# Kernel optimization log

Measured on AMD Instinct MI355X. Metric: run time of the kernel, lower is better.

The kernel has to match this reference:

```python
import jax, jax.numpy as jnp
import numpy as np

B, S, D, P, L, V, C = 8, 4096, 512, 128, 4, 32000, 2
DF = 4 * D      # MLP hidden
DH = D // 2     # head hidden
EPS_LN = 1e-5
EPS_ATTN = 1e-6


def setup_inputs() -> dict:
    key = jax.random.key(0)
    ks = iter(jax.random.split(key, 32))

    def w(shape, fan_in):
        return jax.random.normal(next(ks), shape, jnp.float32) / np.sqrt(fan_in)

    inp = {
        "x": jax.random.randint(next(ks), (B, S), 0, V),
        "embed": jax.random.normal(next(ks), (V, D), jnp.float32) * 0.02,
        "pos": jax.random.normal(next(ks), (S, D), jnp.float32) * 0.02,
        # per-layer params, stacked on leading L axis
        "Wq": w((L, D, D), D), "bq": jnp.zeros((L, D), jnp.float32),
        "Wk": w((L, D, D), D), "bk": jnp.zeros((L, D), jnp.float32),
        "Wv": w((L, D, D), D), "bv": jnp.zeros((L, D), jnp.float32),
        "Wf": w((L, D, P), D), "bf": jnp.zeros((L, P), jnp.float32),
        "Wo": w((L, D, D), D), "bo": jnp.zeros((L, D), jnp.float32),
        "ln_g": jnp.ones((L, D), jnp.float32), "ln_b": jnp.zeros((L, D), jnp.float32),
        "W1": w((L, D, DF), D), "b1": jnp.zeros((L, DF), jnp.float32),
        "W2": w((L, DF, D), DF), "b2": jnp.zeros((L, D), jnp.float32),
        # head
        "Wh1": w((D, DH), D), "bh1": jnp.zeros((DH,), jnp.float32),
        "Wh2": w((DH, C), DH), "bh2": jnp.zeros((C,), jnp.float32),
    }
    return inp


def _layernorm(x, g, b):
    mu = x.mean(-1, keepdims=True)
    var = ((x - mu) ** 2).mean(-1, keepdims=True)
    return (x - mu) * jax.lax.rsqrt(var + EPS_LN) * g + b


def _linear_attn(h, Wq, bq, Wk, bk, Wv, bv, Wf, bf, Wo, bo):
    q = h @ Wq + bq
    k = h @ Wk + bk
    v = h @ Wv + bv
    # positive feature map (Performer-style kernelization) -> [B,S,P]
    pq = jax.nn.elu(q @ Wf + bf) + 1.0
    pk = jax.nn.elu(k @ Wf + bf) + 1.0
    kv = jnp.einsum('bsp,bsd->bpd', pk, v)              # [B,P,D]
    z = jnp.einsum('bsp,bp->bs', pq, pk.sum(axis=1))    # [B,S]
    out = jnp.einsum('bsp,bpd->bsd', pq, kv) / (z[..., None] + EPS_ATTN)
    return out @ Wo + bo


def reference(x, embed, pos, Wq, bq, Wk, bk, Wv, bv, Wf, bf, Wo, bo,
              ln_g, ln_b, W1, b1, W2, b2, Wh1, bh1, Wh2, bh2):
    h = embed[x] + pos[: x.shape[1]]                    # [B,S,D]
    for i in range(L):
        a = _linear_attn(h, Wq[i], bq[i], Wk[i], bk[i], Wv[i], bv[i],
                         Wf[i], bf[i], Wo[i], bo[i])
        a = _layernorm(a, ln_g[i], ln_b[i])
        m = jax.nn.gelu(a @ W1[i] + b1[i])              # [B,S,4D]
        h = m @ W2[i] + b2[i]
    pooled = h.mean(axis=1)                             # [B,D]
    h1 = jax.nn.relu(pooled @ Wh1 + bh1)
    return h1 @ Wh2 + bh2                               # [B,C]
```

## Files before the change

### kernel.cpp

```cpp
#include <hip/hip_runtime.h>

#define B_  8
#define S_  4096
#define D_  512
#define P_  128
#define L_  4
#define DF_ 2048
#define DH_ 256
#define C_  2
#define MTOT (B_*S_)
#define KC_ 8

typedef unsigned short u16;
typedef unsigned int   u32;
typedef short s8v __attribute__((ext_vector_type(8)));
typedef float f4v __attribute__((ext_vector_type(4)));

__device__ __forceinline__ float bf2f(u16 u) {
    return __uint_as_float(((u32)u) << 16);
}
__device__ __forceinline__ u16 f2bf(float f) {
    u32 x = __float_as_uint(f);
    x += 0x7fffu + ((x >> 16) & 1u);
    return (u16)(x >> 16);
}

__device__ __forceinline__ float fast_elu1(float v) {
    return (v > 0.f) ? (v + 1.f) : __expf(v);
}
__device__ __forceinline__ float fast_gelu(float v) {
    float u = 0.7978845608f * (v + 0.044715f * v * v * v);
    return v * __builtin_amdgcn_rcpf(1.f + __expf(-2.f * u));
}
template<int ACT>
__device__ __forceinline__ float act_f(float v) {
    if (ACT == 1) return fast_elu1(v);
    if (ACT == 2) return fast_gelu(v);
    return v;
}

__device__ __forceinline__ void gl2lds16(const u16* g, u16* l) {
    __builtin_amdgcn_global_load_lds(
        (const __attribute__((address_space(1))) u32*)g,
        (__attribute__((address_space(3))) u32*)l, 16, 0, 0);
}

#define MFMA_(d, a, bb) d = __builtin_amdgcn_mfma_f32_16x16x32_bf16(a, bb, d, 0, 0, 0)
#define SB_() __builtin_amdgcn_sched_barrier(0)

__device__ __forceinline__ void swz_bid(int& bx, int& by) {
    const int gx = (int)gridDim.x, gy = (int)gridDim.y;
    const int nwg = gx * gy;
    if (nwg & 7) return;
    int id = by * gx + bx;
    id = (id & 7) * (nwg >> 3) + (id >> 3);
    bx = id % gx; by = id / gx;
}

template<int ACT, int SPLITB>
__global__ __launch_bounds__(512, 2)
void gemm256_k(const u16* __restrict__ A, const u16* __restrict__ Bh,
               const u16* __restrict__ Bl, const float* __restrict__ bias,
               u16* __restrict__ C, int M, int N, int K,
               int br, int sT, long cS, int ldcT)
{
    constexpr int BUF   = SPLITB ? 24576 : 16384;
    constexpr int NLD   = SPLITB ? 6 : 4;
    __shared__ u16 lds[3 * BUF];
    (void)M;

    const int tid  = threadIdx.x;
    int bxs = (int)blockIdx.x, bys = (int)blockIdx.y;
    swz_bid(bxs, bys);
    const int n0   = bxs * 256;
    const int row0 = bys * 256;
    const int b    = (br > 0) ? (row0 / br) : 0;

    const int lane = tid & 63, wave = tid >> 6;
    const int quad = lane >> 4, l16 = lane & 15;
    const int wm = wave >> 2, wn = wave & 3;

    const int srow = lane >> 2;
    const int cswz = (((lane & 3) - ((lane >> 3) & 3)) & 3) * 8;
    const long gA0 = (long)(row0 + wave * 32 + srow) * K + cswz;
    const long gA1 = gA0 + 16 * (long)K;
    const long gB0 = (long)(n0 + wave * 32 + srow) * K + cswz;
    const long gB1 = gB0 + 16 * (long)K;

    const int rq    = ((quad + ((l16 >> 1) & 3)) & 3) * 8;
    const int offA  = (wm * 128 + l16) * 32 + rq;
    const int offBh = 8192  + (wn * 64 + l16) * 32 + rq;
    const int offBl = SPLITB ? (16384 + (wn * 64 + l16) * 32 + rq) : 0;

    f4v acc[8][4];
    #pragma unroll
    for (int i = 0; i < 8; i++)
        #pragma unroll
        for (int j = 0; j < 4; j++)
            acc[i][j] = (f4v){0.f, 0.f, 0.f, 0.f};

    const int NT = K >> 5;

    auto stage_tile = [&](int buf, int kof) {
        u16* d = lds + buf * BUF + wave * 1024;
        gl2lds16(A  + gA0 + kof, d);
        gl2lds16(A  + gA1 + kof, d + 512);
        gl2lds16(Bh + gB0 + kof, d + 8192);
        gl2lds16(Bh + gB1 + kof, d + 8704);
        if (SPLITB) {
            gl2lds16(Bl + gB0 + kof, d + 16384);
            gl2lds16(Bl + gB1 + kof, d + 16896);
        }
    };

    stage_tile(0, 0);
    if (NT > 1) {
        stage_tile(1, 32);
        if (SPLITB) asm volatile("s_waitcnt vmcnt(6)" ::: "memory");
        else        asm volatile("s_waitcnt vmcnt(4)" ::: "memory");
    } else {
        asm volatile("s_waitcnt vmcnt(0)" ::: "memory");
    }
    SB_();
    __builtin_amdgcn_s_barrier();
    SB_();

    s8v a03[4], b01h[2], b01l[2];
    #pragma unroll
    for (int i = 0; i < 4; i++) a03[i] = *(const s8v*)&lds[offA + i * 512];
    #pragma unroll
    for (int j = 0; j < 2; j++) {
        b01h[j] = *(const s8v*)&lds[offBh + j * 512];
        if (SPLITB) b01l[j] = *(const s8v*)&lds[offBl + j * 512];
    }

    int cb = 0;
    for (int t = 0; t < NT; ++t) {
        u16* Lc = lds + cb * BUF;
        const int  nb  = (cb + 2 >= 3) ? (cb - 1) : (cb + 2);
        const bool st  = (t + 2) < NT;
        const int kos = (t + 2) << 5;

        s8v b23h[2], b23l[2], a47[4];
        #pragma unroll
        for (int j = 0; j < 2; j++) {
            b23h[j] = *(const s8v*)&Lc[offBh + (2 + j) * 512];
            if (SPLITB) b23l[j] = *(const s8v*)&Lc[offBl + (2 + j) * 512];
        }
        #pragma unroll
        for (int i = 0; i < 4; i++) a47[i] = *(const s8v*)&Lc[offA + (4 + i) * 512];

        if (st) stage_tile(nb, kos);

        if (SPLITB) asm volatile("s_waitcnt lgkmcnt(8)" ::: "memory");
        else        asm volatile("s_waitcnt lgkmcnt(6)" ::: "memory");
        SB_();
        __builtin_amdgcn_s_setprio(1);
        #pragma unroll
        for (int j = 0; j < 2; j++)
            #pragma unroll
            for (int i = 0; i < 4; i++) MFMA_(acc[i][j], a03[i], b01h[j]);
        if (SPLITB) {
            #pragma unroll
            for (int j = 0; j < 2; j++)
                #pragma unroll
                for (int i = 0; i < 4; i++) MFMA_(acc[i][j], a03[i], b01l[j]);
        }

        asm volatile("s_waitcnt lgkmcnt(4)" ::: "memory");
        SB_();
        #pragma unroll
        for (int j = 0; j < 2; j++)
            #pragma unroll
            for (int i = 0; i < 4; i++) MFMA_(acc[i][2 + j], a03[i], b23h[j]);
        if (SPLITB) {
            #pragma unroll
            for (int j = 0; j < 2; j++)
                #pragma unroll
                for (int i = 0; i < 4; i++) MFMA_(acc[i][2 + j], a03[i], b23l[j]);
        }

        asm volatile("s_waitcnt lgkmcnt(0)" ::: "memory");
        SB_();
        #pragma unroll
        for (int j = 0; j < 2; j++)
            #pragma unroll
            for (int i = 0; i < 4; i++) MFMA_(acc[4 + i][j], a47[i], b01h[j]);
        if (SPLITB) {
            #pragma unroll
            for (int j = 0; j < 2; j++)
                #pragma unroll
                for (int i = 0; i < 4; i++) MFMA_(acc[4 + i][j], a47[i], b01l[j]);
        }
        __builtin_amdgcn_s_setprio(0);

        if (t + 1 < NT) {
            SB_();
            if (st) {
                if (SPLITB) asm volatile("s_waitcnt vmcnt(6)" ::: "memory");
                else        asm volatile("s_waitcnt vmcnt(4)" ::: "memory");
            } else {
                asm volatile("s_waitcnt vmcnt(0)" ::: "memory");
            }
            SB_();
            __builtin_amdgcn_s_barrier();
            SB_();
            const u16* Ln = lds + ((cb + 1 == 3) ? 0 : cb + 1) * BUF;
            #pragma unroll
            for (int i = 0; i < 4; i++) a03[i] = *(const s8v*)&Ln[offA + i * 512];
            #pragma unroll
            for (int j = 0; j < 2; j++) {
                b01h[j] = *(const s8v*)&Ln[offBh + j * 512];
                if (SPLITB) b01l[j] = *(const s8v*)&Ln[offBl + j * 512];
            }
            SB_();
        }
        __builtin_amdgcn_s_setprio(1);
        #pragma unroll
        for (int j = 0; j < 2; j++)
            #pragma unroll
            for (int i = 0; i < 4; i++) MFMA_(acc[4 + i][2 + j], a47[i], b23h[j]);
        if (SPLITB) {
            #pragma unroll
            for (int j = 0; j < 2; j++)
                #pragma unroll
                for (int i = 0; i < 4; i++) MFMA_(acc[4 + i][2 + j], a47[i], b23l[j]);
        }
        __builtin_amdgcn_s_setprio(0);

        cb = (cb + 1 == 3) ? 0 : cb + 1;
    }

    const int sbase = (br > 0) ? (row0 % br) : row0;
    #pragma unroll
    for (int mf = 0; mf < 8; mf++) {
        #pragma unroll
        for (int nf = 0; nf < 4; nf++) {
            const int ng = n0 + wn * 64 + nf * 16 + l16;
            const float bv = bias ? bias[ng] : 0.f;
            float vals[4];
            #pragma unroll
            for (int rg = 0; rg < 4; rg++)
                vals[rg] = act_f<ACT>(acc[mf][nf][rg] + bv);
            if (sT) {
                u32 lo = (u32)f2bf(vals[0]) | ((u32)f2bf(vals[1]) << 16);
                u32 hi = (u32)f2bf(vals[2]) | ((u32)f2bf(vals[3]) << 16);
                uint2 pkd; pkd.x = lo; pkd.y = hi;
                long idx = (long)b * cS + (long)ng * ldcT + sbase + wm * 128 + mf * 16 + quad * 4;
                *(uint2*)&C[idx] = pkd;
            } else {
                #pragma unroll
                for (int rg = 0; rg < 4; rg++)
                    C[(long)(row0 + wm * 128 + mf * 16 + quad * 4 + rg) * N + ng] = f2bf(vals[rg]);
            }
        }
    }
}

template<int ACT, int SPLITB>
__global__ __launch_bounds__(256)
void gemm128_k(const u16* __restrict__ A, const u16* __restrict__ Bh,
               const u16* __restrict__ Bl, const float* __restrict__ bias,
               const float* __restrict__ rowscale,
               u16* __restrict__ C, int M, int N, int K,
               long aS, long bS, int br, int sT, long cS, int ldcT)
{
    __shared__ u16 As [128 * 32];
    __shared__ u16 Bs [128 * 32];
    __shared__ u16 Bls[SPLITB ? 128 * 32 : 64];

    const int tid  = threadIdx.x;
    int bxs = (int)blockIdx.x, bys = (int)blockIdx.y;
    if (gridDim.z == 1) swz_bid(bxs, bys);
    const int n0   = bxs * 128;
    const int row0 = bys * 128;
    const int b    = (gridDim.z > 1) ? (int)blockIdx.z : (br > 0 ? row0 / br : 0);
    const u16* Ab  = A  + (long)b * aS;
    const u16* Bhb = Bh + (long)b * bS;
    const u16* Blb = SPLITB ? (Bl + (long)b * bS) : nullptr;

    const int lane = tid & 63, wave = tid >> 6;
    const int quad = lane >> 4, l16 = lane & 15;
    const int wm = wave >> 1, wn = wave & 1;

    const int c0 = wave * 2, c1 = wave * 2 + 1;
    const int srow = lane >> 2;
    const int scol = (lane & 3) * 8;
    const long gA0 = (long)(row0 + c0 * 16 + srow) * K + scol;
    const long gA1 = (long)(row0 + c1 * 16 + srow) * K + scol;
    const long gB0 = (long)(n0   + c0 * 16 + srow) * K + scol;
    const long gB1 = (long)(n0   + c1 * 16 + srow) * K + scol;
    u16* lA0 = &As [c0 * 512]; u16* lA1 = &As [c1 * 512];
    u16* lB0 = &Bs [c0 * 512]; u16* lB1 = &Bs [c1 * 512];
    u16* lL0 = &Bls[SPLITB ? c0 * 512 : 0];
    u16* lL1 = &Bls[SPLITB ? c1 * 512 : 0];

    f4v acc[4][4];
    #pragma unroll
    for (int i = 0; i < 4; i++)
        #pragma unroll
        for (int j = 0; j < 4; j++)
            acc[i][j] = (f4v){0.f, 0.f, 0.f, 0.f};

    for (int kt = 0; kt < K; kt += 32) {
        gl2lds16(Ab  + gA0 + kt, lA0);
        gl2lds16(Ab  + gA1 + kt, lA1);
        gl2lds16(Bhb + gB0 + kt, lB0);
        gl2lds16(Bhb + gB1 + kt, lB1);
        if (SPLITB) {
            gl2lds16(Blb + gB0 + kt, lL0);
            gl2lds16(Blb + gB1 + kt, lL1);
        }
        __syncthreads();

        s8v af[4], bh[4];
        #pragma unroll
        for (int i = 0; i < 4; i++)
            af[i] = *(const s8v*)&As[(wm * 64 + i * 16 + l16) * 32 + quad * 8];
        #pragma unroll
        for (int j = 0; j < 4; j++)
            bh[j] = *(const s8v*)&Bs[(wn * 64 + j * 16 + l16) * 32 + quad * 8];
        #pragma unroll
        for (int i = 0; i < 4; i++)
            #pragma unroll
            for (int j = 0; j < 4; j++)
                acc[i][j] = __builtin_amdgcn_mfma_f32_16x16x32_bf16(af[i], bh[j], acc[i][j], 0, 0, 0);
        if (SPLITB) {
            s8v bl[4];
            #pragma unroll
            for (int j = 0; j < 4; j++)
                bl[j] = *(const s8v*)&Bls[(wn * 64 + j * 16 + l16) * 32 + quad * 8];
            #pragma unroll
            for (int i = 0; i < 4; i++)
                #pragma unroll
                for (int j = 0; j < 4; j++)
                    acc[i][j] = __builtin_amdgcn_mfma_f32_16x16x32_bf16(af[i], bl[j], acc[i][j], 0, 0, 0);
        }
        __syncthreads();
    }

    const int sbase = (br > 0) ? (row0 % br) : row0;
    #pragma unroll
    for (int i = 0; i < 4; i++) {
        #pragma unroll
        for (int j = 0; j < 4; j++) {
            const int nl = wn * 64 + j * 16 + l16;
            const int ng = n0 + nl;
            const float bv = bias ? bias[ng] : 0.f;
            float vals[4];
            #pragma unroll
            for (int rg = 0; rg < 4; rg++) {
                const int mg = row0 + wm * 64 + i * 16 + quad * 4 + rg;
                float v = act_f<ACT>(acc[i][j][rg] + bv);
                if (rowscale) v *= rowscale[mg];
                vals[rg] = v;
            }
            if (sT) {
                u32 lo = (u32)f2bf(vals[0]) | ((u32)f2bf(vals[1]) << 16);
                u32 hi = (u32)f2bf(vals[2]) | ((u32)f2bf(vals[3]) << 16);
                uint2 pkd; pkd.x = lo; pkd.y = hi;
                long idx = (long)b * cS + (long)ng * ldcT + sbase + wm * 64 + i * 16 + quad * 4;
                *(uint2*)&C[idx] = pkd;
            } else {
                #pragma unroll
                for (int rg = 0; rg < 4; rg++) {
                    const int ml = wm * 64 + i * 16 + quad * 4 + rg;
                    C[(long)(row0 + ml) * N + ng] = f2bf(vals[rg]);
                }
            }
        }
    }
}

__global__ __launch_bounds__(256)
void kvpart_k(const u16* __restrict__ pkT, const u16* __restrict__ vT,
              float* __restrict__ part)
{
    __shared__ u16 As[64 * 32];
    __shared__ u16 Bs[64 * 32];
    const int tid  = threadIdx.x;
    const int n0   = blockIdx.x * 64;
    const int row0 = blockIdx.y * 64;
    const int b    = blockIdx.z >> 3;
    const int kc   = blockIdx.z & 7;
    const u16* Ab = pkT + (long)b * P_ * S_;
    const u16* Bb = vT  + (long)b * D_ * S_;

    const int lane = tid & 63, wave = tid >> 6;
    const int quad = lane >> 4, l16 = lane & 15;
    const int wm = wave >> 1, wn = wave & 1;
    const int srow = lane >> 2, scol = (lane & 3) * 8;
    const long gA = (long)(row0 + wave * 16 + srow) * S_ + scol;
    const long gB = (long)(n0   + wave * 16 + srow) * S_ + scol;
    u16* lA = &As[wave * 512];
    u16* lB = &Bs[wave * 512];

    f4v acc[2][2];
    #pragma unroll
    for (int i = 0; i < 2; i++)
        #pragma unroll
        for (int j = 0; j < 2; j++)
            acc[i][j] = (f4v){0.f, 0.f, 0.f, 0.f};

    const int k0 = kc * (S_ / KC_), k1 = k0 + S_ / KC_;
    for (int kt = k0; kt < k1; kt += 32) {
        gl2lds16(Ab + gA + kt, lA);
        gl2lds16(Bb + gB + kt, lB);
        __syncthreads();
        s8v a0 = *(const s8v*)&As[(wm * 32 + l16) * 32 + quad * 8];
        s8v a1 = *(const s8v*)&As[(wm * 32 + 16 + l16) * 32 + quad * 8];
        s8v b0 = *(const s8v*)&Bs[(wn * 32 + l16) * 32 + quad * 8];
        s8v b1 = *(const s8v*)&Bs[(wn * 32 + 16 + l16) * 32 + quad * 8];
        acc[0][0] = __builtin_amdgcn_mfma_f32_16x16x32_bf16(a0, b0, acc[0][0], 0, 0, 0);
        acc[0][1] = __builtin_amdgcn_mfma_f32_16x16x32_bf16(a0, b1, acc[0][1], 0, 0, 0);
        acc[1][0] = __builtin_amdgcn_mfma_f32_16x16x32_bf16(a1, b0, acc[1][0], 0, 0, 0);
        acc[1][1] = __builtin_amdgcn_mfma_f32_16x16x32_bf16(a1, b1, acc[1][1], 0, 0, 0);
        __syncthreads();
    }

    float* pb = part + ((long)(kc * B_ + b) * P_) * D_;
    #pragma unroll
    for (int i = 0; i < 2; i++) {
        #pragma unroll
        for (int j = 0; j < 2; j++) {
            const int ng = n0 + wn * 32 + j * 16 + l16;
            #pragma unroll
            for (int rg = 0; rg < 4; rg++) {
                const int mg = row0 + wm * 32 + i * 16 + quad * 4 + rg;
                pb[(long)mg * D_ + ng] = acc[i][j][rg];
            }
        }
    }
}

__global__ __launch_bounds__(256)
void kvred_k(const float* __restrict__ part, u16* __restrict__ kvT)
{
    __shared__ float t[32][33];
    const int d0 = blockIdx.x * 32, p0 = blockIdx.y * 32, b = blockIdx.z;
    const int r = threadIdx.x >> 3, c4 = (threadIdx.x & 7) * 4;
    float4 s = {0.f, 0.f, 0.f, 0.f};
    #pragma unroll
    for (int kc = 0; kc < KC_; kc++) {
        const float4 v = *(const float4*)&part[(((long)(kc * B_ + b)) * P_ + p0 + r) * D_ + d0 + c4];
        s.x += v.x; s.y += v.y; s.z += v.z; s.w += v.w;
    }
    t[r][c4 + 0] = s.x; t[r][c4 + 1] = s.y; t[r][c4 + 2] = s.z; t[r][c4 + 3] = s.w;
    __syncthreads();
    u16 o[4];
    #pragma unroll
    for (int i = 0; i < 4; i++) o[i] = f2bf(t[c4 + i][r]);
    uint2 ov; ov.x = (u32)o[0] | ((u32)o[1] << 16); ov.y = (u32)o[2] | ((u32)o[3] << 16);
    *(uint2*)&kvT[(long)b * D_ * P_ + (long)(d0 + r) * P_ + p0 + c4] = ov;
}

__global__ __launch_bounds__(256)
void tsplit_k(const float* __restrict__ W, u16* __restrict__ WhT, u16* __restrict__ WlT,
              int K, int N)
{
    __shared__ float t[32][33];
    const int n0 = blockIdx.x * 32, k0 = blockIdx.y * 32;
    const int tid = threadIdx.x;
    const int r = tid >> 3, c4 = (tid & 7) * 4;
    float4 d = *(const float4*)&W[(long)(k0 + r) * N + n0 + c4];
    t[r][c4 + 0] = d.x; t[r][c4 + 1] = d.y; t[r][c4 + 2] = d.z; t[r][c4 + 3] = d.w;
    __syncthreads();
    u16 hi[4], lo[4];
    #pragma unroll
    for (int i = 0; i < 4; i++) {
        float wv = t[c4 + i][r];
        hi[i] = f2bf(wv);
        lo[i] = f2bf(wv - bf2f(hi[i]));
    }
    uint2 hv; hv.x = (u32)hi[0] | ((u32)hi[1] << 16); hv.y = (u32)hi[2] | ((u32)hi[3] << 16);
    uint2 lv; lv.x = (u32)lo[0] | ((u32)lo[1] << 16); lv.y = (u32)lo[2] | ((u32)lo[3] << 16);
    const long oidx = (long)(n0 + r) * K + k0 + c4;
    *(uint2*)&WhT[oidx] = hv;
    *(uint2*)&WlT[oidx] = lv;
}

__global__ __launch_bounds__(256)
void embed_k(const int* __restrict__ x, const float* __restrict__ emb,
             const float* __restrict__ pos, u16* __restrict__ h)
{
    const long i8 = ((long)blockIdx.x * 256 + threadIdx.x) * 8;
    const int bs = (int)(i8 >> 9);
    const int d  = (int)(i8 & 511);
    const int tok = x[bs];
    const int sp  = bs & (S_ - 1);
    float4 e0 = *(const float4*)&emb[(long)tok * D_ + d];
    float4 e1 = *(const float4*)&emb[(long)tok * D_ + d + 4];
    float4 p0 = *(const float4*)&pos[(long)sp * D_ + d];
    float4 p1 = *(const float4*)&pos[(long)sp * D_ + d + 4];
    float4 ov; u16* ow = (u16*)&ov;
    ow[0] = f2bf(e0.x + p0.x); ow[1] = f2bf(e0.y + p0.y);
    ow[2] = f2bf(e0.z + p0.z); ow[3] = f2bf(e0.w + p0.w);
    ow[4] = f2bf(e1.x + p1.x); ow[5] = f2bf(e1.y + p1.y);
    ow[6] = f2bf(e1.z + p1.z); ow[7] = f2bf(e1.w + p1.w);
    *(float4*)&h[i8] = ov;
}

__global__ __launch_bounds__(64)
void ksum_k(const u16* __restrict__ pkT, float* __restrict__ ks)
{
    const int bp = blockIdx.x;
    const int lane = threadIdx.x;
    const u16* row = pkT + (long)bp * S_;
    float s = 0.f;
    for (int i = lane * 8; i < S_; i += 64 * 8) {
        float4 dv = *(const float4*)&row[i];
        const u16* dw = (const u16*)&dv;
        #pragma unroll
        for (int j = 0; j < 8; j++) s += bf2f(dw[j]);
    }
    #pragma unroll
    for (int off = 32; off; off >>= 1) s += __shfl_down(s, off);
    if (lane == 0) ks[bp] = s;
}

__global__ __launch_bounds__(256)
void zinv_k(const u16* __restrict__ pq, const float* __restrict__ ks, float* __restrict__ zi)
{
    const int row = blockIdx.x * 4 + (threadIdx.x >> 6);
    const int lane = threadIdx.x & 63;
    const u16* pr = pq + (long)row * P_;
    const float* kb = ks + (row >> 12) * P_;
    float s = bf2f(pr[lane]) * kb[lane] + bf2f(pr[lane + 64]) * kb[lane + 64];
    #pragma unroll
    for (int off = 32; off; off >>= 1) s += __shfl_down(s, off);
    if (lane == 0) zi[row] = 1.f / (s + 1e-6f);
}

__global__ __launch_bounds__(256)
void ln_k(u16* __restrict__ x, const float* __restrict__ g, const float* __restrict__ be)
{
    const int row = blockIdx.x * 4 + (threadIdx.x >> 6);
    const int lane = threadIdx.x & 63;
    u16* xr = x + (long)row * D_;
    float4 dv = *(const float4*)&xr[lane * 8];
    const u16* dw = (const u16*)&dv;
    float v[8], s = 0.f, s2 = 0.f;
    #pragma unroll
    for (int i = 0; i < 8; i++) { v[i] = bf2f(dw[i]); s += v[i]; s2 += v[i] * v[i]; }
    #pragma unroll
    for (int off = 32; off; off >>= 1) { s += __shfl_down(s, off); s2 += __shfl_down(s2, off); }
    s = __shfl(s, 0); s2 = __shfl(s2, 0);
    const float mu = s * (1.f / D_);
    const float var = s2 * (1.f / D_) - mu * mu;
    const float inv = rsqrtf(var + 1e-5f);
    float4 ov; u16* ow = (u16*)&ov;
    #pragma unroll
    for (int i = 0; i < 8; i++) {
        const int d = lane * 8 + i;
        ow[i] = f2bf((v[i] - mu) * inv * g[d] + be[d]);
    }
    *(float4*)&xr[lane * 8] = ov;
}

__global__ __launch_bounds__(256)
void zero_k(float* __restrict__ p, int n)
{
    const int i = blockIdx.x * 256 + threadIdx.x;
    if (i < n) p[i] = 0.f;
}

__global__ __launch_bounds__(256)
void pool_k(const u16* __restrict__ h, float* __restrict__ pooled)
{
    const int d = blockIdx.x * 256 + threadIdx.x;
    const int scnk = blockIdx.y, b = blockIdx.z;
    const u16* hb = h + (long)b * S_ * D_;
    float s = 0.f;
    for (int sr = scnk * 256; sr < scnk * 256 + 256; sr++) s += bf2f(hb[(long)sr * D_ + d]);
    atomicAdd(&pooled[b * D_ + d], s * (1.f / S_));
}

__global__ __launch_bounds__(256)
void head_k(const float* __restrict__ pooled, const float* __restrict__ Wh1, const float* __restrict__ bh1,
            const float* __restrict__ Wh2, const float* __restrict__ bh2, float* __restrict__ out)
{
    const int b = blockIdx.x, j = threadIdx.x;
    __shared__ float pl[D_];
    __shared__ float h1[DH_];
    pl[j] = pooled[b * D_ + j];
    pl[j + 256] = pooled[b * D_ + 256 + j];
    __syncthreads();
    float s = bh1[j];
    for (int d = 0; d < D_; d++) s += pl[d] * Wh1[d * DH_ + j];
    h1[j] = s > 0.f ? s : 0.f;
    __syncthreads();
    if (j < C_) {
        float o = bh2[j];
        for (int t = 0; t < DH_; t++) o += h1[t] * Wh2[t * C_ + j];
        out[b * C_ + j] = o;
    }
}

static inline void gemm256(hipStream_t st, int act, int splitb,
                           const u16* A, const u16* Bh, const u16* Bl, const float* bias,
                           u16* C, int M, int N, int K, int br, int sT, long cS, int ldcT)
{
    dim3 g(N / 256, M / 256, 1), blk(512, 1, 1);
    if (splitb) {
        switch (act) {
            case 0: gemm256_k<0,1><<<g, blk, 0, st>>>(A, Bh, Bl, bias, C, M, N, K, br, sT, cS, ldcT); break;
            case 1: gemm256_k<1,1><<<g, blk, 0, st>>>(A, Bh, Bl, bias, C, M, N, K, br, sT, cS, ldcT); break;
            case 2: gemm256_k<2,1><<<g, blk, 0, st>>>(A, Bh, Bl, bias, C, M, N, K, br, sT, cS, ldcT); break;
        }
    } else {
        switch (act) {
            case 0: gemm256_k<0,0><<<g, blk, 0, st>>>(A, Bh, Bl, bias, C, M, N, K, br, sT, cS, ldcT); break;
            case 1: gemm256_k<1,0><<<g, blk, 0, st>>>(A, Bh, Bl, bias, C, M, N, K, br, sT, cS, ldcT); break;
            case 2: gemm256_k<2,0><<<g, blk, 0, st>>>(A, Bh, Bl, bias, C, M, N, K, br, sT, cS, ldcT); break;
        }
    }
}

static inline void gemm128(hipStream_t st, int act, int splitb,
                           const u16* A, const u16* Bh, const u16* Bl, const float* bias,
                           const float* rs, u16* C, int M, int N, int K,
                           long aS, long bS, int br, int sT, long cS, int ldcT, int gz)
{
    dim3 g(N / 128, M / 128, gz), blk(256, 1, 1);
    if (splitb) {
        switch (act) {
            case 0: gemm128_k<0,1><<<g, blk, 0, st>>>(A, Bh, Bl, bias, rs, C, M, N, K, aS, bS, br, sT, cS, ldcT); break;
            case 1: gemm128_k<1,1><<<g, blk, 0, st>>>(A, Bh, Bl, bias, rs, C, M, N, K, aS, bS, br, sT, cS, ldcT); break;
            case 2: gemm128_k<2,1><<<g, blk, 0, st>>>(A, Bh, Bl, bias, rs, C, M, N, K, aS, bS, br, sT, cS, ldcT); break;
        }
    } else {
        switch (act) {
            case 0: gemm128_k<0,0><<<g, blk, 0, st>>>(A, Bh, Bl, bias, rs, C, M, N, K, aS, bS, br, sT, cS, ldcT); break;
            case 1: gemm128_k<1,0><<<g, blk, 0, st>>>(A, Bh, Bl, bias, rs, C, M, N, K, aS, bS, br, sT, cS, ldcT); break;
            case 2: gemm128_k<2,0><<<g, blk, 0, st>>>(A, Bh, Bl, bias, rs, C, M, N, K, aS, bS, br, sT, cS, ldcT); break;
        }
    }
}

extern "C" void kernel_launch(void* const* d_in, const int* in_sizes, int n_in,
                              void* d_out, int out_size, void* d_ws, size_t ws_size,
                              hipStream_t stream)
{
    const int*   x   = (const int*)d_in[0];
    const float* emb = (const float*)d_in[1];
    const float* pos = (const float*)d_in[2];
    const float* Wq  = (const float*)d_in[3];  const float* bq  = (const float*)d_in[4];
    const float* Wk  = (const float*)d_in[5];  const float* bk  = (const float*)d_in[6];
    const float* Wv  = (const float*)d_in[7];  const float* bv  = (const float*)d_in[8];
    const float* Wf  = (const float*)d_in[9];  const float* bfb = (const float*)d_in[10];
    const float* Wo  = (const float*)d_in[11]; const float* bo  = (const float*)d_in[12];
    const float* lng = (const float*)d_in[13]; const float* lnb = (const float*)d_in[14];
    const float* W1  = (const float*)d_in[15]; const float* b1  = (const float*)d_in[16];
    const float* W2  = (const float*)d_in[17]; const float* b2  = (const float*)d_in[18];
    const float* Wh1 = (const float*)d_in[19]; const float* bh1 = (const float*)d_in[20];
    const float* Wh2 = (const float*)d_in[21]; const float* bh2 = (const float*)d_in[22];
    float* out = (float*)d_out;
    (void)in_sizes; (void)n_in; (void)out_size;

    char* w = (char*)d_ws;
    auto alloc = [&](size_t bytes) -> char* {
        char* p = w; w += (bytes + 255) & ~(size_t)255; return p;
    };
    const size_t HBYTES = (size_t)MTOT * D_ * 2;
    u16* h    = (u16*)alloc(HBYTES);
    u16* bufA = (u16*)alloc(HBYTES);
    u16* bufB = (u16*)alloc(HBYTES);
    u16* wsH  = (u16*)alloc((size_t)D_ * D_ * 2);
    u16* wsL  = (u16*)alloc((size_t)D_ * D_ * 2);
    float* pooled = (float*)alloc((size_t)B_ * D_ * 4);
    size_t used = (size_t)(w - (char*)d_ws);
    int mlp_chunk = MTOT;
    while (mlp_chunk > 8192 && used + (size_t)mlp_chunk * DF_ * 2 + 4096 > ws_size)
        mlp_chunk >>= 1;
    u16* bufM = (u16*)alloc((size_t)mlp_chunk * DF_ * 2);
    u16* bufC = bufM;
    char* hov = (char*)h;
    size_t hoff = 0;
    auto halloc = [&](size_t bytes) -> char* {
        char* p = hov + hoff; hoff += (bytes + 255) & ~(size_t)255; return p;
    };
    u16*   pq     = (u16*)  halloc((size_t)MTOT * P_ * 2);
    u16*   pkT    = (u16*)  halloc((size_t)MTOT * P_ * 2);
    u16*   kvT    = (u16*)  halloc((size_t)B_ * D_ * P_ * 2);
    float* ks     = (float*)halloc((size_t)B_ * P_ * 4);
    float* zi     = (float*)halloc((size_t)MTOT * 4);
    float* kvpart = (float*)bufA;
    u16* W1h = bufA;
    u16* W1l = bufA + (size_t)DF_ * D_;
    u16* W2h = bufA + (size_t)2 * DF_ * D_;
    u16* W2l = bufA + (size_t)3 * DF_ * D_;

    embed_k<<<(MTOT * (long)D_) / (256 * 8), 256, 0, stream>>>(x, emb, pos, h);

    for (int l = 0; l < L_; l++) {
        tsplit_k<<<dim3(D_ / 32, D_ / 32), 256, 0, stream>>>(Wq + (size_t)l * D_ * D_, wsH, wsL, D_, D_);
        gemm256(stream, 0, 1, h, wsH, wsL, bq + l * D_, bufA, MTOT, D_, D_, 0, 0, 0, 0);
        tsplit_k<<<dim3(D_ / 32, D_ / 32), 256, 0, stream>>>(Wk + (size_t)l * D_ * D_, wsH, wsL, D_, D_);
        gemm256(stream, 0, 1, h, wsH, wsL, bk + l * D_, bufB, MTOT, D_, D_, 0, 0, 0, 0);
        tsplit_k<<<dim3(D_ / 32, D_ / 32), 256, 0, stream>>>(Wv + (size_t)l * D_ * D_, wsH, wsL, D_, D_);
        gemm256(stream, 0, 1, h, wsH, wsL, bv + l * D_, bufC, MTOT, D_, D_, S_, 1, (long)D_ * S_, S_);
        tsplit_k<<<dim3(P_ / 32, D_ / 32), 256, 0, stream>>>(Wf + (size_t)l * D_ * P_, wsH, wsL, D_, P_);
        gemm128(stream, 1, 1, bufA, wsH, wsL, bfb + l * P_, nullptr, pq,  MTOT, P_, D_, 0, 0, 0,  0, 0, 0, 1);
        gemm128(stream, 1, 1, bufB, wsH, wsL, bfb + l * P_, nullptr, pkT, MTOT, P_, D_, 0, 0, S_, 1, (long)P_ * S_, S_, 1);
        ksum_k<<<B_ * P_, 64, 0, stream>>>(pkT, ks);
        zinv_k<<<MTOT / 4, 256, 0, stream>>>(pq, ks, zi);
        kvpart_k<<<dim3(D_ / 64, P_ / 64, B_ * KC_), 256, 0, stream>>>(pkT, bufC, kvpart);
        kvred_k<<<dim3(D_ / 32, P_ / 32, B_), 256, 0, stream>>>(kvpart, kvT);
        gemm128(stream, 0, 0, pq, kvT, nullptr, nullptr, zi, bufA, MTOT, D_, P_, 0, (long)D_ * P_, S_, 0, 0, 0, 1);
        tsplit_k<<<dim3(D_ / 32, D_ / 32), 256, 0, stream>>>(Wo + (size_t)l * D_ * D_, wsH, wsL, D_, D_);
        gemm256(stream, 0, 1, bufA, wsH, wsL, bo + l * D_, bufB, MTOT, D_, D_, 0, 0, 0, 0);
        ln_k<<<MTOT / 4, 256, 0, stream>>>(bufB, lng + l * D_, lnb + l * D_);
        tsplit_k<<<dim3(DF_ / 32, D_ / 32), 256, 0, stream>>>(W1 + (size_t)l * D_ * DF_, W1h, W1l, D_, DF_);
        tsplit_k<<<dim3(D_ / 32, DF_ / 32), 256, 0, stream>>>(W2 + (size_t)l * DF_ * D_, W2h, W2l, DF_, D_);
        for (int c = 0; c < MTOT / mlp_chunk; c++) {
            const u16* aPtr = bufB + (size_t)c * mlp_chunk * D_;
            gemm256(stream, 2, 0, aPtr, W1h, nullptr, b1 + l * DF_, bufM, mlp_chunk, DF_, D_, 0, 0, 0, 0);
            gemm256(stream, 0, 0, bufM, W2h, nullptr, b2 + l * D_,  h + (size_t)c * mlp_chunk * D_, mlp_chunk, D_, DF_, 0, 0, 0, 0);
        }
    }

    zero_k<<<(B_ * D_ + 255) / 256, 256, 0, stream>>>(pooled, B_ * D_);
    pool_k<<<dim3(D_ / 256, 16, B_), 256, 0, stream>>>(h, pooled);
    head_k<<<B_, 256, 0, stream>>>(pooled, Wh1, bh1, Wh2, bh2, out);
}
```

Baseline: 1.972 ms.

## Fold Wq/Wk into feature map weights to skip Q and K projections

```diff
diff --git a/kernel.cpp b/kernel.cpp
--- a/kernel.cpp
+++ b/kernel.cpp
@@ -57,6 +57,30 @@
     bx = id % gx; by = id / gx;
 }
 
+__global__ __launch_bounds__(256)
+void wcomp_k(const float* __restrict__ Wa , const float* __restrict__ ba,
+             const float* __restrict__ Wf , const float* __restrict__ bf,
+             u16* __restrict__ WTh, u16* __restrict__ WTl, float* __restrict__ bo)
+{
+    const int idx = blockIdx.x * 256 + threadIdx.x;
+    const int p = idx & (P_ - 1);
+    const int i = idx >> 7;
+    float s = 0.f;
+    #pragma unroll 16
+    for (int j = 0; j < D_; j++)
+        s = fmaf(Wa[(long)i * D_ + j], Wf[(long)j * P_ + p], s);
+    const u16 hi = f2bf(s);
+    WTh[(long)p * D_ + i] = hi;
+    WTl[(long)p * D_ + i] = f2bf(s - bf2f(hi));
+    if (idx < P_) {
+        float t = bf[idx];
+        #pragma unroll 16
+        for (int d = 0; d < D_; d++)
+            t = fmaf(ba[d], Wf[(long)d * P_ + idx], t);
+        bo[idx] = t;
+    }
+}
+
 template<int ACT, int SPLITB>
 __global__ __launch_bounds__(512, 2)
 void gemm256_k(const u16* __restrict__ A, const u16* __restrict__ Bh,
@@ -65,7 +89,6 @@
                int br, int sT, long cS, int ldcT)
 {
     constexpr int BUF   = SPLITB ? 24576 : 16384;
-    constexpr int NLD   = SPLITB ? 6 : 4;
     __shared__ u16 lds[3 * BUF];
     (void)M;
 
@@ -667,6 +690,7 @@
     u16* bufB = (u16*)alloc(HBYTES);
     u16* wsH  = (u16*)alloc((size_t)D_ * D_ * 2);
     u16* wsL  = (u16*)alloc((size_t)D_ * D_ * 2);
+    float* fb = (float*)alloc((size_t)2 * P_ * 4);
     float* pooled = (float*)alloc((size_t)B_ * D_ * 4);
     size_t used = (size_t)(w - (char*)d_ws);
     int mlp_chunk = MTOT;
@@ -674,17 +698,13 @@
         mlp_chunk >>= 1;
     u16* bufM = (u16*)alloc((size_t)mlp_chunk * DF_ * 2);
     u16* bufC = bufM;
-    char* hov = (char*)h;
-    size_t hoff = 0;
-    auto halloc = [&](size_t bytes) -> char* {
-        char* p = hov + hoff; hoff += (bytes + 255) & ~(size_t)255; return p;
-    };
-    u16*   pq     = (u16*)  halloc((size_t)MTOT * P_ * 2);
-    u16*   pkT    = (u16*)  halloc((size_t)MTOT * P_ * 2);
-    u16*   kvT    = (u16*)  halloc((size_t)B_ * D_ * P_ * 2);
-    float* ks     = (float*)halloc((size_t)B_ * P_ * 4);
-    float* zi     = (float*)halloc((size_t)MTOT * 4);
-    float* kvpart = (float*)bufA;
+    u16*   pq     = bufA;
+    float* kvpart = (float*)(bufA + (size_t)MTOT * P_);
+    u16*   pkT    = bufB;
+    u16*   kvT    = bufB + (size_t)MTOT * P_;
+    float* ks     = (float*)(kvT + (size_t)B_ * D_ * P_);
+    float* zi     = ks + (size_t)B_ * P_;
+    u16*   attnO  = h;
     u16* W1h = bufA;
     u16* W1l = bufA + (size_t)DF_ * D_;
     u16* W2h = bufA + (size_t)2 * DF_ * D_;
@@ -693,22 +713,23 @@
     embed_k<<<(MTOT * (long)D_) / (256 * 8), 256, 0, stream>>>(x, emb, pos, h);
 
     for (int l = 0; l < L_; l++) {
-        tsplit_k<<<dim3(D_ / 32, D_ / 32), 256, 0, stream>>>(Wq + (size_t)l * D_ * D_, wsH, wsL, D_, D_);
-        gemm256(stream, 0, 1, h, wsH, wsL, bq + l * D_, bufA, MTOT, D_, D_, 0, 0, 0, 0);
-        tsplit_k<<<dim3(D_ / 32, D_ / 32), 256, 0, stream>>>(Wk + (size_t)l * D_ * D_, wsH, wsL, D_, D_);
-        gemm256(stream, 0, 1, h, wsH, wsL, bk + l * D_, bufB, MTOT, D_, D_, 0, 0, 0, 0);
+        const float* Wf_l = Wf + (size_t)l * D_ * P_;
+        const float* bf_l = bfb + (size_t)l * P_;
+        wcomp_k<<<256, 256, 0, stream>>>(Wq + (size_t)l * D_ * D_, bq + (size_t)l * D_,
+                                         Wf_l, bf_l, wsH, wsL, fb);
+        gemm128(stream, 1, 1, h, wsH, wsL, fb, nullptr, pq, MTOT, P_, D_, 0, 0, 0, 0, 0, 0, 1);
+        wcomp_k<<<256, 256, 0, stream>>>(Wk + (size_t)l * D_ * D_, bk + (size_t)l * D_,
+                                         Wf_l, bf_l, wsH, wsL, fb + P_);
+        gemm128(stream, 1, 1, h, wsH, wsL, fb + P_, nullptr, pkT, MTOT, P_, D_, 0, 0, S_, 1, (long)P_ * S_, S_, 1);
         tsplit_k<<<dim3(D_ / 32, D_ / 32), 256, 0, stream>>>(Wv + (size_t)l * D_ * D_, wsH, wsL, D_, D_);
         gemm256(stream, 0, 1, h, wsH, wsL, bv + l * D_, bufC, MTOT, D_, D_, S_, 1, (long)D_ * S_, S_);
-        tsplit_k<<<dim3(P_ / 32, D_ / 32), 256, 0, stream>>>(Wf + (size_t)l * D_ * P_, wsH, wsL, D_, P_);
-        gemm128(stream, 1, 1, bufA, wsH, wsL, bfb + l * P_, nullptr, pq,  MTOT, P_, D_, 0, 0, 0,  0, 0, 0, 1);
-        gemm128(stream, 1, 1, bufB, wsH, wsL, bfb + l * P_, nullptr, pkT, MTOT, P_, D_, 0, 0, S_, 1, (long)P_ * S_, S_, 1);
         ksum_k<<<B_ * P_, 64, 0, stream>>>(pkT, ks);
         zinv_k<<<MTOT / 4, 256, 0, stream>>>(pq, ks, zi);
         kvpart_k<<<dim3(D_ / 64, P_ / 64, B_ * KC_), 256, 0, stream>>>(pkT, bufC, kvpart);
         kvred_k<<<dim3(D_ / 32, P_ / 32, B_), 256, 0, stream>>>(kvpart, kvT);
-        gemm128(stream, 0, 0, pq, kvT, nullptr, nullptr, zi, bufA, MTOT, D_, P_, 0, (long)D_ * P_, S_, 0, 0, 0, 1);
+        gemm128(stream, 0, 0, pq, kvT, nullptr, nullptr, zi, attnO, MTOT, D_, P_, 0, (long)D_ * P_, S_, 0, 0, 0, 1);
         tsplit_k<<<dim3(D_ / 32, D_ / 32), 256, 0, stream>>>(Wo + (size_t)l * D_ * D_, wsH, wsL, D_, D_);
-        gemm256(stream, 0, 1, bufA, wsH, wsL, bo + l * D_, bufB, MTOT, D_, D_, 0, 0, 0, 0);
+        gemm256(stream, 0, 1, attnO, wsH, wsL, bo + l * D_, bufB, MTOT, D_, D_, 0, 0, 0, 0);
         ln_k<<<MTOT / 4, 256, 0, stream>>>(bufB, lng + l * D_, lnb + l * D_);
         tsplit_k<<<dim3(DF_ / 32, D_ / 32), 256, 0, stream>>>(W1 + (size_t)l * D_ * DF_, W1h, W1l, D_, DF_);
         tsplit_k<<<dim3(D_ / 32, DF_ / 32), 256, 0, stream>>>(W2 + (size_t)l * DF_ * D_, W2h, W2l, DF_, D_);
```

New measurement: 1.929 ms. -2.1%, faster.
